# Performance work log

Hardware: AMD Instinct MI355X
Metric: run time of the kernel (lower is better)

The kernel has to match this reference:

```python
import jax, jax.numpy as jnp
import numpy as np

OUT, IN = 4096, 4096
GROUP_SIZE = 64
NUM_GROUPS = IN // GROUP_SIZE  # 64


def dequantize(packed, mn, scale):
    # packed: [OUT, NUM_GROUPS, GROUP_SIZE//2] int32, byte values 0..255.
    # 4-bit asymmetric layout (torch compress): high nibble holds the first
    # half of each group, low nibble the second half.
    hi = (packed >> 4) & 0xF                      # [OUT, G, 32]
    lo = packed & 0xF                             # [OUT, G, 32]
    vals = jnp.concatenate([hi, lo], axis=-1).astype(jnp.float32)  # [OUT, G, 64]
    w = vals / scale + mn                         # scale, mn broadcast [OUT, G, 1]
    return w.reshape(OUT, IN)


def setup_inputs() -> dict:
    key = jax.random.key(0)
    k1, k2, k3, k4, k5 = jax.random.split(key, 5)
    x = jax.random.normal(k1, (4, 2048, IN), dtype=jnp.float32)
    packed = jax.random.randint(k2, (OUT, NUM_GROUPS, GROUP_SIZE // 2), 0, 256, dtype=jnp.int32)
    mn = jax.random.normal(k3, (OUT, NUM_GROUPS, 1), dtype=jnp.float32) * 0.02
    # scale = B / (mx - mn) is positive; keep it away from zero.
    scale = jax.random.uniform(k4, (OUT, NUM_GROUPS, 1), dtype=jnp.float32) * 200.0 + 100.0
    bias = jax.random.normal(k5, (OUT,), dtype=jnp.float32) * 0.02
    return {"x": x, "packed": packed, "mn": mn, "scale": scale, "bias": bias}


def reference(x, packed, mn, scale, bias):
    w = dequantize(packed, mn, scale)             # [OUT, IN] fp32
    # F.linear: out = x @ w.T + bias
    return jnp.einsum('bsk,nk->bsn', x, w) + bias
```

## Files before the change

### kernel.cpp

```cpp
#include <hip/hip_runtime.h>

typedef unsigned short u16;
typedef __bf16 bf16x8 __attribute__((ext_vector_type(8)));
typedef float f32x4 __attribute__((ext_vector_type(4)));
typedef u16 u16x8 __attribute__((ext_vector_type(8)));

#define M_DIM 8192
#define N_DIM 4096
#define K_DIM 4096

__device__ __forceinline__ u16 f2bf(float f) {
  unsigned int u = __float_as_uint(f);
  u += 0x7fffu + ((u >> 16) & 1u);
  return (u16)(u >> 16);
}

__global__ __launch_bounds__(256) void dequant_kernel(
    const int* __restrict__ packed, const float* __restrict__ mn,
    const float* __restrict__ scale, u16* __restrict__ W) {
  int idx = blockIdx.x * 256 + threadIdx.x;
  int j = idx & 31;
  int g = (idx >> 5) & 63;
  int n = idx >> 11;
  int p = packed[idx];
  float inv = 1.0f / scale[(n << 6) + g];
  float m = mn[(n << 6) + g];
  float hi = (float)((p >> 4) & 0xF) * inv + m;
  float lo = (float)(p & 0xF) * inv + m;
  int base = (n << 12) + (g << 6) + j;
  W[base] = f2bf(hi);
  W[base + 32] = f2bf(lo);
}

__global__ __launch_bounds__(256) void cvt_kernel(const float4* __restrict__ x,
                                                  u16x8* __restrict__ xb) {
  int i = blockIdx.x * 256 + threadIdx.x;
  float4 a = x[2 * i];
  float4 b = x[2 * i + 1];
  u16x8 o;
  o[0] = f2bf(a.x); o[1] = f2bf(a.y); o[2] = f2bf(a.z); o[3] = f2bf(a.w);
  o[4] = f2bf(b.x); o[5] = f2bf(b.y); o[6] = f2bf(b.z); o[7] = f2bf(b.w);
  xb[i] = o;
}

__device__ __forceinline__ void gload_lds16(const u16* g, u16* l) {
  __builtin_amdgcn_global_load_lds(
      (const __attribute__((address_space(1))) void*)g,
      (__attribute__((address_space(3))) void*)l, 16, 0, 0);
}

__global__ __launch_bounds__(256) void gemm_kernel(
    const u16* __restrict__ A,
    const u16* __restrict__ B,
    const float* __restrict__ bias,
    float* __restrict__ C) {
  __shared__ alignas(16) u16 As[128 * 32];
  __shared__ alignas(16) u16 Bs[128 * 32];

  const int tid = threadIdx.x;
  const int wave = tid >> 6;
  const int lane = tid & 63;
  const int lr = lane & 15;
  const int lq = lane >> 4;

  const int bn = blockIdx.x & 31;
  const int bm = blockIdx.x >> 5;
  const int m0 = bm << 7;
  const int n0 = bn << 7;

  const int wm = (wave & 1) << 6;
  const int wn = (wave >> 1) << 6;

  const int off0 = (wave << 10) + (lane << 4);
  const int srow = off0 >> 6;
  const int scol = (off0 & 63) >> 1;

  const u16* gA = A + (size_t)(m0 + srow) * K_DIM + scol;
  const u16* gB = B + (size_t)(n0 + srow) * K_DIM + scol;
  u16* ldsA0 = As + ((wave << 10) >> 1);
  u16* ldsB0 = Bs + ((wave << 10) >> 1);

  f32x4 acc[4][4] = {};

  for (int k0 = 0; k0 < K_DIM; k0 += 32) {
    gload_lds16(gA + k0, ldsA0);
    gload_lds16(gA + (size_t)64 * K_DIM + k0, ldsA0 + 2048);
    gload_lds16(gB + k0, ldsB0);
    gload_lds16(gB + (size_t)64 * K_DIM + k0, ldsB0 + 2048);
    __syncthreads();

    bf16x8 af[4], bfr[4];
#pragma unroll
    for (int i = 0; i < 4; i++)
      af[i] = *(const bf16x8*)(As + (wm + i * 16 + lr) * 32 + lq * 8);
#pragma unroll
    for (int j = 0; j < 4; j++)
      bfr[j] = *(const bf16x8*)(Bs + (wn + j * 16 + lr) * 32 + lq * 8);
#pragma unroll
    for (int i = 0; i < 4; i++)
#pragma unroll
      for (int j = 0; j < 4; j++)
        acc[i][j] = __builtin_amdgcn_mfma_f32_16x16x32_bf16(af[i], bfr[j],
                                                            acc[i][j], 0, 0, 0);
    __syncthreads();
  }

#pragma unroll
  for (int j = 0; j < 4; j++) {
    int n = n0 + wn + j * 16 + lr;
    float bv = bias[n];
#pragma unroll
    for (int i = 0; i < 4; i++) {
      int mb = m0 + wm + i * 16 + lq * 4;
#pragma unroll
      for (int t = 0; t < 4; t++)
        C[(size_t)(mb + t) * N_DIM + n] = acc[i][j][t] + bv;
    }
  }
}

__global__ __launch_bounds__(256) void fallback_gemm(
    const float* __restrict__ x, const int* __restrict__ packed,
    const float* __restrict__ mn, const float* __restrict__ scale,
    const float* __restrict__ bias, float* __restrict__ out) {
  __shared__ float As[16][17];
  __shared__ float Bs[16][17];
  int tx = threadIdx.x & 15, ty = threadIdx.x >> 4;
  int m = blockIdx.y * 16 + ty;
  int n = blockIdx.x * 16 + tx;
  float acc = 0.f;
  for (int k0 = 0; k0 < K_DIM; k0 += 16) {
    As[ty][tx] = x[(size_t)m * K_DIM + k0 + tx];
    int nn = blockIdx.x * 16 + ty;
    int k = k0 + tx;
    int g = k >> 6, pos = k & 63;
    int p = packed[nn * 2048 + g * 32 + (pos & 31)];
    int v = (pos < 32) ? ((p >> 4) & 0xF) : (p & 0xF);
    Bs[ty][tx] = (float)v / scale[nn * 64 + g] + mn[nn * 64 + g];
    __syncthreads();
#pragma unroll
    for (int kk = 0; kk < 16; kk++) acc += As[ty][kk] * Bs[tx][kk];
    __syncthreads();
  }
  out[(size_t)m * N_DIM + n] = acc + bias[n];
}

extern "C" void kernel_launch(void* const* d_in, const int* in_sizes, int n_in,
                              void* d_out, int out_size, void* d_ws, size_t ws_size,
                              hipStream_t stream) {
  const float* x = (const float*)d_in[0];
  const int* packed = (const int*)d_in[1];
  const float* mn = (const float*)d_in[2];
  const float* scale = (const float*)d_in[3];
  const float* bias = (const float*)d_in[4];
  float* out = (float*)d_out;

  const size_t needW = (size_t)N_DIM * K_DIM * 2;
  const size_t needX = (size_t)M_DIM * K_DIM * 2;

  if (ws_size >= needW + needX) {
    u16* W = (u16*)d_ws;
    u16* Xb = (u16*)((char*)d_ws + needW);
    dequant_kernel<<<(N_DIM * 64 * 32) / 256, 256, 0, stream>>>(packed, mn,
                                                                scale, W);
    cvt_kernel<<<(size_t)M_DIM * K_DIM / (256 * 8), 256, 0, stream>>>(
        (const float4*)x, (u16x8*)Xb);
    gemm_kernel<<<(M_DIM / 128) * (N_DIM / 128), 256, 0, stream>>>(Xb, W, bias,
                                                                   out);
  } else {
    dim3 grid(N_DIM / 16, M_DIM / 16);
    fallback_gemm<<<grid, 256, 0, stream>>>(x, packed, mn, scale, bias, out);
  }
}
```

Baseline: 551.8 us.

## Fuse dequant and input conversion into one launch; double K step per GEMM barrier

Merges the weight dequantization and the fp32-to-bf16 input conversion into a single prep kernel, with the block index choosing which job a block does. This removes one kernel launch, but each conversion thread now handles 4 floats instead of 8. The GEMM main loop now loads two 32-wide K slices into doubled LDS buffers before each barrier pair, which halves the number of __syncthreads per tile. This doubles LDS use per block and may reduce occupancy.

```diff
diff --git a/kernel.cpp b/kernel.cpp
--- a/kernel.cpp
+++ b/kernel.cpp
@@ -3,7 +3,6 @@
 typedef unsigned short u16;
 typedef __bf16 bf16x8 __attribute__((ext_vector_type(8)));
 typedef float f32x4 __attribute__((ext_vector_type(4)));
-typedef u16 u16x8 __attribute__((ext_vector_type(8)));
 
 #define M_DIM 8192
 #define N_DIM 4096
@@ -15,32 +14,32 @@
   return (u16)(u >> 16);
 }
 
-__global__ __launch_bounds__(256) void dequant_kernel(
+#define DQ_BLOCKS 32768
+__global__ __launch_bounds__(256) void prep_kernel(
     const int* __restrict__ packed, const float* __restrict__ mn,
-    const float* __restrict__ scale, u16* __restrict__ W) {
-  int idx = blockIdx.x * 256 + threadIdx.x;
-  int j = idx & 31;
-  int g = (idx >> 5) & 63;
-  int n = idx >> 11;
-  int p = packed[idx];
-  float inv = 1.0f / scale[(n << 6) + g];
-  float m = mn[(n << 6) + g];
-  float hi = (float)((p >> 4) & 0xF) * inv + m;
-  float lo = (float)(p & 0xF) * inv + m;
-  int base = (n << 12) + (g << 6) + j;
-  W[base] = f2bf(hi);
-  W[base + 32] = f2bf(lo);
-}
-
-__global__ __launch_bounds__(256) void cvt_kernel(const float4* __restrict__ x,
-                                                  u16x8* __restrict__ xb) {
-  int i = blockIdx.x * 256 + threadIdx.x;
-  float4 a = x[2 * i];
-  float4 b = x[2 * i + 1];
-  u16x8 o;
-  o[0] = f2bf(a.x); o[1] = f2bf(a.y); o[2] = f2bf(a.z); o[3] = f2bf(a.w);
-  o[4] = f2bf(b.x); o[5] = f2bf(b.y); o[6] = f2bf(b.z); o[7] = f2bf(b.w);
-  xb[i] = o;
+    const float* __restrict__ scale, u16* __restrict__ W,
+    const float4* __restrict__ x, ushort4* __restrict__ xb) {
+  int b = blockIdx.x;
+  if (b < DQ_BLOCKS) {
+    int idx = b * 256 + threadIdx.x;
+    int j = idx & 31;
+    int g = (idx >> 5) & 63;
+    int n = idx >> 11;
+    int p = packed[idx];
+    float inv = 1.0f / scale[(n << 6) + g];
+    float m = mn[(n << 6) + g];
+    float hi = (float)((p >> 4) & 0xF) * inv + m;
+    float lo = (float)(p & 0xF) * inv + m;
+    int base = (n << 12) + (g << 6) + j;
+    W[base] = f2bf(hi);
+    W[base + 32] = f2bf(lo);
+  } else {
+    int i = (b - DQ_BLOCKS) * 256 + threadIdx.x;
+    float4 a = x[i];
+    ushort4 o;
+    o.x = f2bf(a.x); o.y = f2bf(a.y); o.z = f2bf(a.z); o.w = f2bf(a.w);
+    xb[i] = o;
+  }
 }
 
 __device__ __forceinline__ void gload_lds16(const u16* g, u16* l) {
@@ -54,8 +53,8 @@
     const u16* __restrict__ B,
     const float* __restrict__ bias,
     float* __restrict__ C) {
-  __shared__ alignas(16) u16 As[128 * 32];
-  __shared__ alignas(16) u16 Bs[128 * 32];
+  __shared__ alignas(16) u16 As[2 * 128 * 32];
+  __shared__ alignas(16) u16 Bs[2 * 128 * 32];
 
   const int tid = threadIdx.x;
   const int wave = tid >> 6;
@@ -77,31 +76,40 @@
 
   const u16* gA = A + (size_t)(m0 + srow) * K_DIM + scol;
   const u16* gB = B + (size_t)(n0 + srow) * K_DIM + scol;
-  u16* ldsA0 = As + ((wave << 10) >> 1);
-  u16* ldsB0 = Bs + ((wave << 10) >> 1);
+  u16* ldsA0 = As + (wave << 9);
+  u16* ldsB0 = Bs + (wave << 9);
 
   f32x4 acc[4][4] = {};
 
-  for (int k0 = 0; k0 < K_DIM; k0 += 32) {
+  for (int k0 = 0; k0 < K_DIM; k0 += 64) {
     gload_lds16(gA + k0, ldsA0);
     gload_lds16(gA + (size_t)64 * K_DIM + k0, ldsA0 + 2048);
     gload_lds16(gB + k0, ldsB0);
     gload_lds16(gB + (size_t)64 * K_DIM + k0, ldsB0 + 2048);
+    gload_lds16(gA + k0 + 32, ldsA0 + 4096);
+    gload_lds16(gA + (size_t)64 * K_DIM + k0 + 32, ldsA0 + 6144);
+    gload_lds16(gB + k0 + 32, ldsB0 + 4096);
+    gload_lds16(gB + (size_t)64 * K_DIM + k0 + 32, ldsB0 + 6144);
     __syncthreads();
 
-    bf16x8 af[4], bfr[4];
 #pragma unroll
-    for (int i = 0; i < 4; i++)
-      af[i] = *(const bf16x8*)(As + (wm + i * 16 + lr) * 32 + lq * 8);
+    for (int s = 0; s < 2; s++) {
+      const u16* as = As + s * 4096;
+      const u16* bs = Bs + s * 4096;
+      bf16x8 af[4], bfr[4];
 #pragma unroll
-    for (int j = 0; j < 4; j++)
-      bfr[j] = *(const bf16x8*)(Bs + (wn + j * 16 + lr) * 32 + lq * 8);
-#pragma unroll
-    for (int i = 0; i < 4; i++)
+      for (int i = 0; i < 4; i++)
+        af[i] = *(const bf16x8*)(as + (wm + i * 16 + lr) * 32 + lq * 8);
 #pragma unroll
       for (int j = 0; j < 4; j++)
-        acc[i][j] = __builtin_amdgcn_mfma_f32_16x16x32_bf16(af[i], bfr[j],
-                                                            acc[i][j], 0, 0, 0);
+        bfr[j] = *(const bf16x8*)(bs + (wn + j * 16 + lr) * 32 + lq * 8);
+#pragma unroll
+      for (int i = 0; i < 4; i++)
+#pragma unroll
+        for (int j = 0; j < 4; j++)
+          acc[i][j] = __builtin_amdgcn_mfma_f32_16x16x32_bf16(
+              af[i], bfr[j], acc[i][j], 0, 0, 0);
+    }
     __syncthreads();
   }
 
@@ -161,10 +169,9 @@
   if (ws_size >= needW + needX) {
     u16* W = (u16*)d_ws;
     u16* Xb = (u16*)((char*)d_ws + needW);
-    dequant_kernel<<<(N_DIM * 64 * 32) / 256, 256, 0, stream>>>(packed, mn,
-                                                                scale, W);
-    cvt_kernel<<<(size_t)M_DIM * K_DIM / (256 * 8), 256, 0, stream>>>(
-        (const float4*)x, (u16x8*)Xb);
+    const int cvt_blocks = (int)((size_t)M_DIM * K_DIM / 4 / 256);
+    prep_kernel<<<DQ_BLOCKS + cvt_blocks, 256, 0, stream>>>(
+        packed, mn, scale, W, (const float4*)x, (ushort4*)Xb);
     gemm_kernel<<<(M_DIM / 128) * (N_DIM / 128), 256, 0, stream>>>(Xb, W, bias,
                                                                    out);
   } else {
```

Result: faster. 529.2 us (-4.1%).
